# Optimization experiments

Measured on AMD Instinct MI355X. Metric: run time of the kernel, lower is better.

The kernel has to match this reference:

```python
import jax, jax.numpy as jnp
import numpy as np

NUM_HEADS = 8
GROUPS = 32
EPS = 1e-5


def group_norm(x, gamma, beta):
    # x: [B, C, H, W], normalize over (C/G, H, W) per group
    B, C, H, W = x.shape
    xg = x.reshape(B, GROUPS, -1)
    mu = xg.mean(axis=-1, keepdims=True)
    var = xg.var(axis=-1, keepdims=True)
    xg = (xg - mu) * jax.lax.rsqrt(var + EPS)
    x = xg.reshape(B, C, H, W)
    return x * gamma[None, :, None, None] + beta[None, :, None, None]


def reference(x, w_qkv, w_out, b_out, temperature, g1, beta1, g2, beta2,
              w_mlp1, b_mlp1, w_mlp2, b_mlp2):
    B, C, H, W = x.shape
    hd = C // NUM_HEADS
    N = H * W
    identity = x

    xn = group_norm(x, g1, beta1)
    # 1x1 conv == per-pixel matmul
    qkv = jnp.einsum('oc,bchw->bohw', w_qkv, xn)  # [B, 3C, H, W]
    q, k, v = jnp.split(qkv, 3, axis=1)
    q = q.reshape(B, NUM_HEADS, hd, N)
    k = k.reshape(B, NUM_HEADS, hd, N)
    v = v.reshape(B, NUM_HEADS, hd, N)

    temp = jnp.clip(temperature, 1e-4, 10.0)  # [heads,1,1]
    attn = jnp.einsum('bhdi,bhdj->bhij', q, k) * temp[None]  # [B,h,N,N]
    attn = jax.nn.softmax(attn, axis=-1)  # max-subtract is folded into stable softmax

    out = jnp.einsum('bhdj,bhij->bhdi', v, attn)  # [B,h,hd,N]
    out = out.reshape(B, C, H, W)
    out = jnp.einsum('oc,bchw->bohw', w_out, out) + b_out[None, :, None, None]
    x = identity + out

    y = group_norm(x, g2, beta2)
    h = jnp.einsum('oc,bchw->bohw', w_mlp1, y) + b_mlp1[None, :, None, None]
    h = jax.nn.gelu(h, approximate=False)
    m = jnp.einsum('oc,bchw->bohw', w_mlp2, h) + b_mlp2[None, :, None, None]
    return x + m


def setup_inputs() -> dict:
    key = jax.random.key(0)
    ks = jax.random.split(key, 8)
    C = 256
    B, H, W = 2, 64, 64
    hid = C // 4
    s_in = 1.0 / np.sqrt(C)
    s_hid = 1.0 / np.sqrt(hid)
    return {
        'x': jax.random.normal(ks[0], (B, C, H, W), jnp.float32),
        'w_qkv': jax.random.normal(ks[1], (3 * C, C), jnp.float32) * s_in,
        'w_out': jax.random.normal(ks[2], (C, C), jnp.float32) * s_in,
        'b_out': jnp.zeros((C,), jnp.float32),
        'temperature': jnp.ones((NUM_HEADS, 1, 1), jnp.float32) * (C // NUM_HEADS) ** -0.5,
        'g1': jnp.ones((C,), jnp.float32),
        'beta1': jnp.zeros((C,), jnp.float32),
        'g2': jnp.ones((C,), jnp.float32),
        'beta2': jnp.zeros((C,), jnp.float32),
        'w_mlp1': jax.random.normal(ks[3], (hid, C), jnp.float32) * s_in,
        'b_mlp1': jnp.zeros((hid,), jnp.float32),
        'w_mlp2': jax.random.normal(ks[4], (C, hid), jnp.float32) * s_hid,
        'b_mlp2': jnp.zeros((C,), jnp.float32),
    }
```

## Files before the change

### kernel.cpp

```cpp
#include <hip/hip_runtime.h>
#include <hip/hip_bf16.h>
#include <math.h>

#define NB 2
#define NC 256
#define NHEAD 8
#define HD 32
#define NPIX 4096
#define GEPS 1e-5f
#define NCHUNK 2
#define JLEN (NPIX / NCHUNK)

typedef short bf16x8 __attribute__((ext_vector_type(8)));
typedef float f32x4 __attribute__((ext_vector_type(4)));

typedef __attribute__((address_space(3))) unsigned int lds_u32;
typedef __attribute__((address_space(1))) const unsigned int glb_u32;

union U16x8 { uint4 u4; uint2 u2[2]; unsigned u32[4]; unsigned short us[8]; bf16x8 v; };

__device__ inline unsigned short tobf(float f) {
  union { float f; unsigned u; } c; c.f = f;
  return (unsigned short)((c.u + 0x7FFFu + ((c.u >> 16) & 1u)) >> 16);
}
__device__ inline unsigned packtrunc(float lo, float hi) {
  return __builtin_amdgcn_perm(__float_as_uint(hi), __float_as_uint(lo), 0x07060302u);
}
__device__ inline float geluf(float v) {
  return 0.5f * v * (1.f + erff(v * 0.70710678118654752f));
}

__device__ inline int detect_bf(const void* xraw) {
  __shared__ int flg;
  int t = threadIdx.x;
  if (t < 64) {
    unsigned short h = ((const unsigned short*)xraw)[2 * t];
    unsigned e = (h >> 7) & 0xFFu;
    int weird = (e < 113u || e > 140u) ? 1 : 0;
    unsigned long long m = __ballot(weird);
    if (t == 0) flg = (__popcll(m) > 16) ? 0 : 1;
  }
  __syncthreads();
  return flg;
}

struct ConvArgs { const void* src[13]; int off[14]; };

__device__ inline float ldsrc(const void* p, int idx, int bf) {
  if (bf) {
    unsigned v = ((const unsigned short*)p)[idx];
    return __uint_as_float(v << 16);
  }
  return ((const float*)p)[idx];
}

__global__ __launch_bounds__(256) void conv_prep_kernel(
    ConvArgs a, float* __restrict__ dstbase, int total,
    unsigned short* __restrict__ wqkv_b, unsigned short* __restrict__ wout_b,
    unsigned short* __restrict__ wm1_b, unsigned short* __restrict__ wm2_b,
    float* __restrict__ qscale, float* __restrict__ part1p) {
  int bf = detect_bf(a.src[0]);
  int blk = blockIdx.x, t = threadIdx.x;
  int i = blk * 256 + t;
  float val = 0.f;
  if (i < total) {
    int s = 0;
    while (i >= a.off[s + 1]) ++s;
    val = ldsrc(a.src[s], i - a.off[s], bf);
    dstbase[i] = val;
  }
  if (blk < 8192) {
    __shared__ float rs[256], rq[256];
    rs[t] = val;
    rq[t] = val * val;
    __syncthreads();
    for (int o = 128; o > 0; o >>= 1) {
      if (t < o) { rs[t] += rs[t + o]; rq[t] += rq[t + o]; }
      __syncthreads();
    }
    if (t == 0) { part1p[blk * 2] = rs[0]; part1p[blk * 2 + 1] = rq[0]; }
  }
  if (i < 196608) wqkv_b[i] = tobf(ldsrc(a.src[1], i, bf));
  else if (i < 262144) wout_b[i - 196608] = tobf(ldsrc(a.src[2], i - 196608, bf));
  else if (i < 278528) wm1_b[i - 262144] = tobf(ldsrc(a.src[9], i - 262144, bf));
  else if (i < 294912) wm2_b[i - 278528] = tobf(ldsrc(a.src[11], i - 278528, bf));
  if (i < 768) {
    if (i < 256) {
      float tc = fminf(fmaxf(ldsrc(a.src[4], i >> 5, bf), 1e-4f), 10.f);
      qscale[i] = tc * 1.4426950408889634f;
    } else qscale[i] = 1.0f;
  }
}

__global__ __launch_bounds__(256) void qkv_fused_kernel(
    const float* __restrict__ x_f, const float* __restrict__ part1p,
    const float* __restrict__ g1, const float* __restrict__ be1,
    const unsigned short* __restrict__ W, const float* __restrict__ qscale,
    unsigned short* __restrict__ qn, unsigned short* __restrict__ kn,
    unsigned short* __restrict__ vs) {
  int t = threadIdx.x;
  int w = t >> 6, lane = t & 63, l16 = lane & 15, quad = lane >> 4;
  int p0 = blockIdx.x * 16;
  int b = p0 >> 12;
  __shared__ float red[32][8][2];
  __shared__ float sm[32], si[32];
  {
    int g = t >> 3, seg = t & 7;
    float s = 0.f, s2 = 0.f;
    const float* pp = part1p + ((size_t)(b * 32 + g) * 128 + seg * 16) * 2;
#pragma unroll
    for (int k = 0; k < 16; ++k) { s += pp[k * 2]; s2 += pp[k * 2 + 1]; }
    red[g][seg][0] = s; red[g][seg][1] = s2;
  }
  __syncthreads();
  if (t < 32) {
    float s = 0.f, s2 = 0.f;
#pragma unroll
    for (int k = 0; k < 8; ++k) { s += red[t][k][0]; s2 += red[t][k][1]; }
    float mean = s * (1.f / 32768.f);
    float var = s2 * (1.f / 32768.f) - mean * mean;
    sm[t] = mean; si[t] = rsqrtf(var + GEPS);
  }
  __syncthreads();
  __shared__ unsigned short Ys[16][264];
  {
    int p = t & 15, cg = t >> 4;
    int n = (p0 & 4095) + p;
    const float* src = x_f + ((size_t)b * NC + cg * 16) * NPIX + n;
    U16x8 lo, hi;
#pragma unroll
    for (int cc = 0; cc < 16; ++cc) {
      int c = cg * 16 + cc;
      int g = c >> 3;
      float gg = g1[c] * si[g];
      float vv = (src[(size_t)cc * NPIX] - sm[g]) * gg + be1[c];
      if (cc < 8) lo.us[cc] = tobf(vv); else hi.us[cc - 8] = tobf(vv);
    }
    *(uint4*)&Ys[p][cg * 16] = lo.u4;
    *(uint4*)&Ys[p][cg * 16 + 8] = hi.u4;
  }
  __syncthreads();
  int ob = blockIdx.y * 384 + w * 96;
  f32x4 acc[6] = {};
#pragma unroll
  for (int k0 = 0; k0 < 256; k0 += 32) {
    U16x8 bfr; bfr.u4 = *(const uint4*)&Ys[l16][k0 + quad * 8];
#pragma unroll
    for (int ot = 0; ot < 6; ++ot) {
      U16x8 af;
      af.u4 = *(const uint4*)(W + (size_t)(ob + ot * 16 + l16) * 256 + k0 + quad * 8);
      acc[ot] = __builtin_amdgcn_mfma_f32_16x16x32_bf16(af.v, bfr.v, acc[ot], 0, 0, 0);
    }
  }
  int n = (p0 & 4095) + l16;
#pragma unroll
  for (int ot = 0; ot < 6; ++ot) {
    int oc = ob + ot * 16 + quad * 4;
    float v[4];
#pragma unroll
    for (int r = 0; r < 4; ++r) v[r] = acc[ot][r] * qscale[oc + r];
    int sec = oc >> 8;
    int c = oc & 255;
    if (sec < 2) {
      int hh = c >> 5, d = c & 31;
      unsigned short* base = sec == 0 ? qn : kn;
      uint2 pk;
      pk.x = (unsigned)tobf(v[0]) | ((unsigned)tobf(v[1]) << 16);
      pk.y = (unsigned)tobf(v[2]) | ((unsigned)tobf(v[3]) << 16);
      *(uint2*)(base + ((size_t)(b * NHEAD + hh) * NPIX + n) * HD + d) = pk;
    } else {
#pragma unroll
      for (int r = 0; r < 4; ++r)
        vs[((size_t)(b * NC + c + r)) * NPIX + n] = tobf(v[r]);
    }
  }
}

__global__ __launch_bounds__(512) void attn11_kernel(
    const unsigned short* __restrict__ qn, const unsigned short* __restrict__ kn,
    const unsigned short* __restrict__ vs, float* __restrict__ pO,
    float* __restrict__ pl) {
  int f = blockIdx.x;
  int xcd = f & 7, slot = f >> 3;
  int s = xcd + ((slot >> 5) << 3);
  int iblk = slot & 31;
  int chunk = s & 1;
  int h = (s >> 1) & 7;
  int b = s >> 4;
  int i0 = iblk * 128;
  int jbase = chunk * JLEN;
  int bh = b * NHEAD + h;
  int t = threadIdx.x;
  int w = t >> 6, lane = t & 63, l16 = lane & 15, quad = lane >> 4;

  __shared__ unsigned short Kt[2][2048];
  __shared__ unsigned short Vt[2][2048];
  __shared__ unsigned short Pl[8][16][72];

  U16x8 qf;
  qf.u4 = *(const uint4*)(qn + ((size_t)bh * NPIX + i0 + w * 16 + l16) * HD + quad * 8);
  U16x8 ones;
#pragma unroll
  for (int j = 0; j < 8; ++j) ones.us[j] = 0x3F80;

  const unsigned short* gp;
  lds_u32* dstN[2];
  if (w < 4) {
    int kj = (w << 4) + (lane >> 2);
    int kg = (lane & 3) ^ ((kj >> 1) & 3);
    gp = kn + ((size_t)bh * NPIX + jbase + kj) * HD + kg * 8;
    dstN[0] = (lds_u32*)&Kt[0][w * 512];
    dstN[1] = (lds_u32*)&Kt[1][w * 512];
  } else {
    int vd = ((w - 4) << 3) + (lane >> 3);
    int vg = (lane & 7) ^ (vd & 7);
    gp = vs + ((size_t)(b * NC + h * HD + vd)) * NPIX + jbase + vg * 8;
    dstN[0] = (lds_u32*)&Vt[0][(w - 4) * 512];
    dstN[1] = (lds_u32*)&Vt[1][(w - 4) * 512];
  }
  int gstep = (w < 4) ? 64 * HD : 64;

  f32x4 o0 = {0.f, 0.f, 0.f, 0.f}, o1 = {0.f, 0.f, 0.f, 0.f};
  f32x4 lacc = {0.f, 0.f, 0.f, 0.f};
  const f32x4 zf = {0.f, 0.f, 0.f, 0.f};

  int sp = (quad ^ ((l16 >> 1) & 3)) * 8;

  __builtin_amdgcn_global_load_lds((glb_u32*)gp, dstN[0], 16, 0, 0);
  gp += gstep;

#define ATTN_STEP(CUR, ISSUE)                                                   \
  {                                                                             \
    asm volatile("s_waitcnt vmcnt(0)" ::: "memory");                            \
    __builtin_amdgcn_s_barrier();                                               \
    if (ISSUE) {                                                                \
      __builtin_amdgcn_global_load_lds((glb_u32*)gp, dstN[(CUR) ^ 1], 16, 0, 0);\
      gp += gstep;                                                              \
    }                                                                           \
    __builtin_amdgcn_sched_barrier(0);                                          \
    f32x4 st[4];                                                                \
    __builtin_amdgcn_s_setprio(1);                                              \
    _Pragma("unroll")                                                           \
    for (int jj = 0; jj < 4; ++jj) {                                            \
      U16x8 kf; kf.u4 = *(const uint4*)&Kt[CUR][(jj * 16 + l16) * 32 + sp];     \
      st[jj] = __builtin_amdgcn_mfma_f32_16x16x32_bf16(kf.v, qf.v, zf, 0, 0, 0);\
    }                                                                           \
    __builtin_amdgcn_s_setprio(0);                                              \
    _Pragma("unroll")                                                           \
    for (int jj = 0; jj < 4; ++jj) {                                            \
      uint2 pk;                                                                 \
      pk.x = packtrunc(__builtin_amdgcn_exp2f(st[jj][0]),                       \
                       __builtin_amdgcn_exp2f(st[jj][1]));                      \
      pk.y = packtrunc(__builtin_amdgcn_exp2f(st[jj][2]),                       \
                       __builtin_amdgcn_exp2f(st[jj][3]));                      \
      *(uint2*)&Pl[w][l16][jj * 16 + quad * 4] = pk;                            \
    }                                                                           \
    __builtin_amdgcn_s_setprio(1);                                              \
    _Pragma("unroll")                                                           \
    for (int ks = 0; ks < 2; ++ks) {                                            \
      U16x8 pb; pb.u4 = *(const uint4*)&Pl[w][l16][ks * 32 + quad * 8];         \
      int vp = ((ks * 4 + quad) ^ (l16 & 7)) * 8;                               \
      U16x8 va; va.u4 = *(const uint4*)&Vt[CUR][l16 * 64 + vp];                 \
      U16x8 vb2; vb2.u4 = *(const uint4*)&Vt[CUR][(16 + l16) * 64 + vp];        \
      o0 = __builtin_amdgcn_mfma_f32_16x16x32_bf16(va.v, pb.v, o0, 0, 0, 0);    \
      o1 = __builtin_amdgcn_mfma_f32_16x16x32_bf16(vb2.v, pb.v, o1, 0, 0, 0);   \
      lacc = __builtin_amdgcn_mfma_f32_16x16x32_bf16(ones.v, pb.v, lacc, 0, 0, 0);\
    }                                                                           \
    __builtin_amdgcn_s_setprio(0);                                              \
  }

#pragma unroll 1
  for (int it = 0; it < 15; ++it) {
    ATTN_STEP(0, 1)
    ATTN_STEP(1, 1)
  }
  ATTN_STEP(0, 1)
  ATTN_STEP(1, 0)
#undef ATTN_STEP

  int pr = bh * 64 + iblk * 2 + (w >> 2);
  float* ob = pO + ((size_t)chunk * 1024 + pr) * 2048;
  int icol = (w & 3) * 16 + l16;
#pragma unroll
  for (int r = 0; r < 4; ++r) {
    ob[(quad * 4 + r) * 64 + icol] = o0[r];
    ob[(16 + quad * 4 + r) * 64 + icol] = o1[r];
  }
  if (quad == 0)
    pl[((size_t)chunk * 1024 + pr) * 64 + icol] = lacc[0];
}

__global__ __launch_bounds__(256) void wout_kernel(
    const unsigned short* __restrict__ W, const float* __restrict__ pO,
    const float* __restrict__ pl, const float* __restrict__ bias,
    const float* __restrict__ res, float* __restrict__ xres_t,
    float* __restrict__ part2p) {
  int t = threadIdx.x;
  int w = t >> 6, lane = t & 63, l16 = lane & 15, quad = lane >> 4;
  int p = blockIdx.x * 16 + l16;
  int b = p >> 12, n = p & 4095;
  int i = p & 63, iblk = (p >> 6) & 63;
  int ob = w * 64;
  float rinv8[8];
#pragma unroll
  for (int hh = 0; hh < 8; ++hh) {
    size_t pr = (size_t)(b * NHEAD + hh) * 64 + iblk;
    float l = pl[pr * 64 + i] + pl[(1024 + pr) * 64 + i];
    rinv8[hh] = 1.f / l;
  }
  f32x4 acc[4] = {};
#pragma unroll
  for (int k0 = 0; k0 < 256; k0 += 32) {
    int hh = k0 >> 5;
    const float* q0 = pO + ((size_t)(b * NHEAD + hh) * 64 + iblk) * 2048 + quad * 8 * 64 + i;
    const float* q1 = q0 + (size_t)1024 * 2048;
    float rv = rinv8[hh];
    U16x8 bfr;
#pragma unroll
    for (int u = 0; u < 4; ++u) {
      float va = (q0[(2 * u) * 64] + q1[(2 * u) * 64]) * rv;
      float vb = (q0[(2 * u + 1) * 64] + q1[(2 * u + 1) * 64]) * rv;
      bfr.u32[u] = packtrunc(va, vb);
    }
#pragma unroll
    for (int ot = 0; ot < 4; ++ot) {
      U16x8 af;
      af.u4 = *(const uint4*)(W + (size_t)(ob + ot * 16 + l16) * 256 + k0 + quad * 8);
      acc[ot] = __builtin_amdgcn_mfma_f32_16x16x32_bf16(af.v, bfr.v, acc[ot], 0, 0, 0);
    }
  }
  __shared__ float sb[256][4][2];
#pragma unroll
  for (int ot = 0; ot < 4; ++ot) {
    int oc = ob + ot * 16 + quad * 4;
    float s = 0.f, s2 = 0.f;
    float v4[4];
#pragma unroll
    for (int r = 0; r < 4; ++r) {
      float vv = acc[ot][r] + bias[oc + r] + res[((size_t)(b * NC + oc + r)) * NPIX + n];
      v4[r] = vv;
      s += vv; s2 += vv * vv;
    }
    *(float4*)&xres_t[(size_t)p * NC + oc] = make_float4(v4[0], v4[1], v4[2], v4[3]);
    sb[t][ot][0] = s; sb[t][ot][1] = s2;
  }
  __syncthreads();
  if (t < 32) {
    int ww = t >> 3, rem = t & 7, ot = rem >> 1, qp = rem & 1;
    float s = 0.f, s2 = 0.f;
#pragma unroll
    for (int q = 2 * qp; q < 2 * qp + 2; ++q)
      for (int l = 0; l < 16; ++l) {
        int tt = ww * 64 + q * 16 + l;
        s += sb[tt][ot][0]; s2 += sb[tt][ot][1];
      }
    size_t idx = ((size_t)(b * 32 + t) * 256 + (blockIdx.x & 255)) * 2;
    part2p[idx] = s; part2p[idx + 1] = s2;
  }
}

__global__ __launch_bounds__(256) void mlp_fused_kernel(
    const void* __restrict__ xraw, const float* __restrict__ xres_t,
    const float* __restrict__ part2p, const float* __restrict__ g2,
    const float* __restrict__ be2, const unsigned short* __restrict__ W1,
    const float* __restrict__ b1, const unsigned short* __restrict__ W2,
    const float* __restrict__ b2, void* __restrict__ dout) {
  int wbf = detect_bf(xraw);
  int t = threadIdx.x;
  int w = t >> 6, lane = t & 63, l16 = lane & 15, quad = lane >> 4;
  int p0 = blockIdx.x * 16;
  int b = p0 >> 12;
  __shared__ float red[32][8][2];
  __shared__ float sm[32], si[32];
  {
    int g = t >> 3, seg = t & 7;
    float s = 0.f, s2 = 0.f;
    const float* pp = part2p + ((size_t)(b * 32 + g) * 256 + seg * 32) * 2;
#pragma unroll
    for (int k = 0; k < 32; ++k) { s += pp[k * 2]; s2 += pp[k * 2 + 1]; }
    red[g][seg][0] = s; red[g][seg][1] = s2;
  }
  __syncthreads();
  if (t < 32) {
    float s = 0.f, s2 = 0.f;
#pragma unroll
    for (int k = 0; k < 8; ++k) { s += red[t][k][0]; s2 += red[t][k][1]; }
    float mean = s * (1.f / 32768.f);
    float var = s2 * (1.f / 32768.f) - mean * mean;
    sm[t] = mean; si[t] = rsqrtf(var + GEPS);
  }
  __syncthreads();
  __shared__ float Xs[16][261];
  __shared__ unsigned short Ys[16][264];
  {
    int p = t >> 4, cg = t & 15;
    const float* src = xres_t + (size_t)(p0 + p) * NC + cg * 16;
    U16x8 lo, hi;
#pragma unroll
    for (int cc = 0; cc < 16; ++cc) {
      int c = cg * 16 + cc;
      int g = c >> 3;
      float v = src[cc];
      Xs[p][c] = v;
      float yv = (v - sm[g]) * (g2[c] * si[g]) + be2[c];
      if (cc < 8) lo.us[cc] = tobf(yv); else hi.us[cc - 8] = tobf(yv);
    }
    *(uint4*)&Ys[p][cg * 16] = lo.u4;
    *(uint4*)&Ys[p][cg * 16 + 8] = hi.u4;
  }
  __syncthreads();
  f32x4 a1 = {0.f, 0.f, 0.f, 0.f};
#pragma unroll
  for (int k0 = 0; k0 < 256; k0 += 32) {
    U16x8 bfr; bfr.u4 = *(const uint4*)&Ys[l16][k0 + quad * 8];
    U16x8 af;
    af.u4 = *(const uint4*)(W1 + (size_t)(w * 16 + l16) * 256 + k0 + quad * 8);
    a1 = __builtin_amdgcn_mfma_f32_16x16x32_bf16(af.v, bfr.v, a1, 0, 0, 0);
  }
  __shared__ unsigned short Hs[16][72];
  {
    int oc = w * 16 + quad * 4;
    float h0 = geluf(a1[0] + b1[oc]),     h1 = geluf(a1[1] + b1[oc + 1]);
    float h2 = geluf(a1[2] + b1[oc + 2]), h3 = geluf(a1[3] + b1[oc + 3]);
    uint2 pk;
    pk.x = (unsigned)tobf(h0) | ((unsigned)tobf(h1) << 16);
    pk.y = (unsigned)tobf(h2) | ((unsigned)tobf(h3) << 16);
    *(uint2*)&Hs[l16][oc] = pk;
  }
  __syncthreads();
  f32x4 a2[4] = {};
#pragma unroll
  for (int k0 = 0; k0 < 64; k0 += 32) {
    U16x8 bfr; bfr.u4 = *(const uint4*)&Hs[l16][k0 + quad * 8];
#pragma unroll
    for (int ot = 0; ot < 4; ++ot) {
      U16x8 af;
      af.u4 = *(const uint4*)(W2 + (size_t)(w * 64 + ot * 16 + l16) * 64 + k0 + quad * 8);
      a2[ot] = __builtin_amdgcn_mfma_f32_16x16x32_bf16(af.v, bfr.v, a2[ot], 0, 0, 0);
    }
  }
  int n = (p0 & 4095) + l16;
#pragma unroll
  for (int ot = 0; ot < 4; ++ot) {
    int oc = w * 64 + ot * 16 + quad * 4;
#pragma unroll
    for (int r = 0; r < 4; ++r) {
      float v = a2[ot][r] + b2[oc + r] + Xs[l16][oc + r];
      size_t oidx = ((size_t)(b * NC + oc + r)) * NPIX + n;
      if (wbf) ((__hip_bfloat16*)dout)[oidx] = __float2bfloat16(v);
      else ((float*)dout)[oidx] = v;
    }
  }
}

extern "C" void kernel_launch(void* const* d_in, const int* in_sizes, int n_in,
                              void* d_out, int out_size, void* d_ws, size_t ws_size,
                              hipStream_t stream) {
  float* ws = (float*)d_ws;
  size_t off = 16;
  float* x_f    = ws + off; off += (size_t)NB * NC * NPIX;
  float* wqkv_f = ws + off; off += 768 * 256;
  float* wout_f = ws + off; off += 256 * 256;
  float* bout_f = ws + off; off += 256;
  float* temp_f = ws + off; off += 8;
  float* g1_f   = ws + off; off += 256;
  float* be1_f  = ws + off; off += 256;
  float* g2_f   = ws + off; off += 256;
  float* be2_f  = ws + off; off += 256;
  float* wm1_f  = ws + off; off += 64 * 256;
  float* bm1_f  = ws + off; off += 64;
  float* wm2_f  = ws + off; off += 256 * 64;
  float* bm2_f  = ws + off; off += 256;
  float* xres   = ws + off; off += (size_t)NB * NC * NPIX;
  unsigned short* qn     = (unsigned short*)(ws + off); off += 1048576;
  unsigned short* kn     = (unsigned short*)(ws + off); off += 1048576;
  unsigned short* vs     = (unsigned short*)(ws + off); off += 1048576;
  unsigned short* wqkv_b = (unsigned short*)(ws + off); off += 98304;
  unsigned short* wout_b = (unsigned short*)(ws + off); off += 32768;
  unsigned short* wm1_b  = (unsigned short*)(ws + off); off += 8192;
  unsigned short* wm2_b  = (unsigned short*)(ws + off); off += 8192;
  float* qscale = ws + off; off += 768;
  float* part1p = ws + off; off += 16384;
  float* part2p = ws + off; off += 65536;
  float* pO     = ws + off; off += (size_t)NCHUNK * 1024 * 2048;
  float* plb    = ws + off; off += (size_t)NCHUNK * 1024 * 64;
  (void)wqkv_f; (void)wout_f; (void)wm1_f; (void)wm2_f; (void)temp_f; (void)bm1_f;

  ConvArgs ca;
  int acc = 0;
  for (int i = 0; i < 13; ++i) {
    ca.src[i] = d_in[i];
    ca.off[i] = acc;
    acc += (i < n_in) ? in_sizes[i] : 0;
  }
  ca.off[13] = acc;
  conv_prep_kernel<<<(acc + 255) / 256, 256, 0, stream>>>(
      ca, x_f, acc, wqkv_b, wout_b, wm1_b, wm2_b, qscale, part1p);

  qkv_fused_kernel<<<dim3(512, 2), 256, 0, stream>>>(
      x_f, part1p, g1_f, be1_f, wqkv_b, qscale, qn, kn, vs);

  attn11_kernel<<<dim3(1024), 512, 0, stream>>>(qn, kn, vs, pO, plb);

  wout_kernel<<<512, 256, 0, stream>>>(wout_b, pO, plb, bout_f, x_f, xres, part2p);

  mlp_fused_kernel<<<512, 256, 0, stream>>>(
      d_in[0], xres, part2p, g2_f, be2_f, wm1_b, bm1_f, wm2_b, bm2_f, d_out);
}
```

Measured before the change: 210.6 us.

## Software-pipeline attention: overlap QK^T of next tile with PV of previous

Restructures the attention inner loop so each step computes QK^T scores for the current K tile while running the PV MFMAs for the previous tile's probabilities held in registers. K and V loads are staggered by one stage, with K prefetched a tile ahead and V loaded into the current buffer, and an epilogue drains the final PV. The aim is to hide exp2 and pack latency behind matrix work and shorten the dependency chain per step. It adds register pressure from carrying the packed P across iterations and depends on the buffer-index bookkeeping being correct.

```diff
diff --git a/kernel.cpp b/kernel.cpp
--- a/kernel.cpp
+++ b/kernel.cpp
@@ -176,7 +176,7 @@
   }
 }
 
-__global__ __launch_bounds__(512) void attn11_kernel(
+__global__ __launch_bounds__(512) void attn12_kernel(
     const unsigned short* __restrict__ qn, const unsigned short* __restrict__ kn,
     const unsigned short* __restrict__ vs, float* __restrict__ pO,
     float* __restrict__ pl) {
@@ -223,60 +223,83 @@
   f32x4 o0 = {0.f, 0.f, 0.f, 0.f}, o1 = {0.f, 0.f, 0.f, 0.f};
   f32x4 lacc = {0.f, 0.f, 0.f, 0.f};
   const f32x4 zf = {0.f, 0.f, 0.f, 0.f};
+  uint2 pk[4];
 
   int sp = (quad ^ ((l16 >> 1) & 3)) * 8;
 
-  __builtin_amdgcn_global_load_lds((glb_u32*)gp, dstN[0], 16, 0, 0);
-  gp += gstep;
-
-#define ATTN_STEP(CUR, ISSUE)                                                   \
+  if (w < 4) {
+    __builtin_amdgcn_global_load_lds((glb_u32*)gp, dstN[0], 16, 0, 0);
+    gp += gstep;
+  }
+
+#define ATTN_STEP(P, DOPV)                                                      \
   {                                                                             \
     asm volatile("s_waitcnt vmcnt(0)" ::: "memory");                            \
     __builtin_amdgcn_s_barrier();                                               \
-    if (ISSUE) {                                                                \
-      __builtin_amdgcn_global_load_lds((glb_u32*)gp, dstN[(CUR) ^ 1], 16, 0, 0);\
+    {                                                                           \
+      lds_u32* d_ = (w < 4) ? dstN[(P) ^ 1] : dstN[(P)];                        \
+      __builtin_amdgcn_global_load_lds((glb_u32*)gp, d_, 16, 0, 0);             \
       gp += gstep;                                                              \
     }                                                                           \
     __builtin_amdgcn_sched_barrier(0);                                          \
+    if (DOPV) {                                                                 \
+      _Pragma("unroll")                                                         \
+      for (int jj = 0; jj < 4; ++jj)                                            \
+        *(uint2*)&Pl[w][l16][jj * 16 + quad * 4] = pk[jj];                      \
+    }                                                                           \
     f32x4 st[4];                                                                \
     __builtin_amdgcn_s_setprio(1);                                              \
     _Pragma("unroll")                                                           \
     for (int jj = 0; jj < 4; ++jj) {                                            \
-      U16x8 kf; kf.u4 = *(const uint4*)&Kt[CUR][(jj * 16 + l16) * 32 + sp];     \
+      U16x8 kf; kf.u4 = *(const uint4*)&Kt[P][(jj * 16 + l16) * 32 + sp];       \
       st[jj] = __builtin_amdgcn_mfma_f32_16x16x32_bf16(kf.v, qf.v, zf, 0, 0, 0);\
+    }                                                                           \
+    if (DOPV) {                                                                 \
+      _Pragma("unroll")                                                         \
+      for (int ks = 0; ks < 2; ++ks) {                                          \
+        U16x8 pb; pb.u4 = *(const uint4*)&Pl[w][l16][ks * 32 + quad * 8];       \
+        int vp = ((ks * 4 + quad) ^ (l16 & 7)) * 8;                             \
+        U16x8 va; va.u4 = *(const uint4*)&Vt[(P) ^ 1][l16 * 64 + vp];           \
+        U16x8 vb2; vb2.u4 = *(const uint4*)&Vt[(P) ^ 1][(16 + l16) * 64 + vp];  \
+        o0 = __builtin_amdgcn_mfma_f32_16x16x32_bf16(va.v, pb.v, o0, 0, 0, 0);  \
+        o1 = __builtin_amdgcn_mfma_f32_16x16x32_bf16(vb2.v, pb.v, o1, 0, 0, 0); \
+        lacc = __builtin_amdgcn_mfma_f32_16x16x32_bf16(ones.v, pb.v, lacc, 0, 0, 0);\
+      }                                                                         \
     }                                                                           \
     __builtin_amdgcn_s_setprio(0);                                              \
     _Pragma("unroll")                                                           \
     for (int jj = 0; jj < 4; ++jj) {                                            \
-      uint2 pk;                                                                 \
-      pk.x = packtrunc(__builtin_amdgcn_exp2f(st[jj][0]),                       \
-                       __builtin_amdgcn_exp2f(st[jj][1]));                      \
-      pk.y = packtrunc(__builtin_amdgcn_exp2f(st[jj][2]),                       \
-                       __builtin_amdgcn_exp2f(st[jj][3]));                      \
-      *(uint2*)&Pl[w][l16][jj * 16 + quad * 4] = pk;                            \
+      pk[jj].x = packtrunc(__builtin_amdgcn_exp2f(st[jj][0]),                   \
+                           __builtin_amdgcn_exp2f(st[jj][1]));                  \
+      pk[jj].y = packtrunc(__builtin_amdgcn_exp2f(st[jj][2]),                   \
+                           __builtin_amdgcn_exp2f(st[jj][3]));                  \
     }                                                                           \
-    __builtin_amdgcn_s_setprio(1);                                              \
-    _Pragma("unroll")                                                           \
-    for (int ks = 0; ks < 2; ++ks) {                                            \
-      U16x8 pb; pb.u4 = *(const uint4*)&Pl[w][l16][ks * 32 + quad * 8];         \
-      int vp = ((ks * 4 + quad) ^ (l16 & 7)) * 8;                               \
-      U16x8 va; va.u4 = *(const uint4*)&Vt[CUR][l16 * 64 + vp];                 \
-      U16x8 vb2; vb2.u4 = *(const uint4*)&Vt[CUR][(16 + l16) * 64 + vp];        \
-      o0 = __builtin_amdgcn_mfma_f32_16x16x32_bf16(va.v, pb.v, o0, 0, 0, 0);    \
-      o1 = __builtin_amdgcn_mfma_f32_16x16x32_bf16(vb2.v, pb.v, o1, 0, 0, 0);   \
-      lacc = __builtin_amdgcn_mfma_f32_16x16x32_bf16(ones.v, pb.v, lacc, 0, 0, 0);\
-    }                                                                           \
-    __builtin_amdgcn_s_setprio(0);                                              \
-  }
-
+  }
+
+  ATTN_STEP(0, 0)
+  ATTN_STEP(1, 1)
 #pragma unroll 1
   for (int it = 0; it < 15; ++it) {
     ATTN_STEP(0, 1)
     ATTN_STEP(1, 1)
   }
-  ATTN_STEP(0, 1)
-  ATTN_STEP(1, 0)
 #undef ATTN_STEP
+
+  asm volatile("s_waitcnt vmcnt(0)" ::: "memory");
+  __builtin_amdgcn_s_barrier();
+#pragma unroll
+  for (int jj = 0; jj < 4; ++jj)
+    *(uint2*)&Pl[w][l16][jj * 16 + quad * 4] = pk[jj];
+#pragma unroll
+  for (int ks = 0; ks < 2; ++ks) {
+    U16x8 pb; pb.u4 = *(const uint4*)&Pl[w][l16][ks * 32 + quad * 8];
+    int vp = ((ks * 4 + quad) ^ (l16 & 7)) * 8;
+    U16x8 va; va.u4 = *(const uint4*)&Vt[1][l16 * 64 + vp];
+    U16x8 vb2; vb2.u4 = *(const uint4*)&Vt[1][(16 + l16) * 64 + vp];
+    o0 = __builtin_amdgcn_mfma_f32_16x16x32_bf16(va.v, pb.v, o0, 0, 0, 0);
+    o1 = __builtin_amdgcn_mfma_f32_16x16x32_bf16(vb2.v, pb.v, o1, 0, 0, 0);
+    lacc = __builtin_amdgcn_mfma_f32_16x16x32_bf16(ones.v, pb.v, lacc, 0, 0, 0);
+  }
 
   int pr = bh * 64 + iblk * 2 + (w >> 2);
   float* ob = pO + ((size_t)chunk * 1024 + pr) * 2048;
@@ -500,7 +523,7 @@
   qkv_fused_kernel<<<dim3(512, 2), 256, 0, stream>>>(
       x_f, part1p, g1_f, be1_f, wqkv_b, qscale, qn, kn, vs);
 
-  attn11_kernel<<<dim3(1024), 512, 0, stream>>>(qn, kn, vs, pO, plb);
+  attn12_kernel<<<dim3(1024), 512, 0, stream>>>(qn, kn, vs, pO, plb);
 
   wout_kernel<<<512, 256, 0, stream>>>(wout_b, pO, plb, bout_f, x_f, xres, part2p);
 
```

New measurement: 211.5 us. No clear change (+0.4%).

## Rewrite attention with 32x32x16 MFMA and register-resident P via permlane swap

Applied to the files above, without the earlier changes.

The attention kernel moves from 16x16x32 MFMA tiles with 8 waves to 32x32x16 MFMA tiles with 4 waves, each wave covering 32 query rows. The softmax probabilities are now converted in registers with v_permlane32_swap instead of being written to and read back from an LDS staging buffer, which removes the Pl shared array and its LDS traffic. K and V loads are now issued by every wave rather than split between wave groups. The trade-offs are fewer waves per block, higher register pressure from the 16-wide accumulators, and a new LDS access pattern without the previous XOR swizzle, which may cause bank conflicts.

```diff
diff --git a/kernel.cpp b/kernel.cpp
--- a/kernel.cpp
+++ b/kernel.cpp
@@ -13,6 +13,7 @@
 
 typedef short bf16x8 __attribute__((ext_vector_type(8)));
 typedef float f32x4 __attribute__((ext_vector_type(4)));
+typedef float f32x16 __attribute__((ext_vector_type(16)));
 
 typedef __attribute__((address_space(3))) unsigned int lds_u32;
 typedef __attribute__((address_space(1))) const unsigned int glb_u32;
@@ -28,6 +29,9 @@
 }
 __device__ inline float geluf(float v) {
   return 0.5f * v * (1.f + erff(v * 0.70710678118654752f));
+}
+__device__ inline void plane32(unsigned &a, unsigned &b) {
+  asm("v_permlane32_swap_b32 %0, %1" : "+v"(a), "+v"(b));
 }
 
 __device__ inline int detect_bf(const void* xraw) {
@@ -176,7 +180,7 @@
   }
 }
 
-__global__ __launch_bounds__(512) void attn11_kernel(
+__global__ __launch_bounds__(256) void attn15_kernel(
     const unsigned short* __restrict__ qn, const unsigned short* __restrict__ kn,
     const unsigned short* __restrict__ vs, float* __restrict__ pO,
     float* __restrict__ pl) {
@@ -191,80 +195,102 @@
   int jbase = chunk * JLEN;
   int bh = b * NHEAD + h;
   int t = threadIdx.x;
-  int w = t >> 6, lane = t & 63, l16 = lane & 15, quad = lane >> 4;
+  int w = t >> 6, lane = t & 63;
+  int q = lane & 31, lh = lane >> 5;
 
   __shared__ unsigned short Kt[2][2048];
   __shared__ unsigned short Vt[2][2048];
-  __shared__ unsigned short Pl[8][16][72];
-
-  U16x8 qf;
-  qf.u4 = *(const uint4*)(qn + ((size_t)bh * NPIX + i0 + w * 16 + l16) * HD + quad * 8);
+
+  int px = i0 + w * 32 + q;
+  U16x8 qf0, qf1;
+  qf0.u4 = *(const uint4*)(qn + ((size_t)bh * NPIX + px) * HD + lh * 8);
+  qf1.u4 = *(const uint4*)(qn + ((size_t)bh * NPIX + px) * HD + 16 + lh * 8);
   U16x8 ones;
 #pragma unroll
   for (int j = 0; j < 8; ++j) ones.us[j] = 0x3F80;
 
-  const unsigned short* gp;
-  lds_u32* dstN[2];
-  if (w < 4) {
-    int kj = (w << 4) + (lane >> 2);
-    int kg = (lane & 3) ^ ((kj >> 1) & 3);
-    gp = kn + ((size_t)bh * NPIX + jbase + kj) * HD + kg * 8;
-    dstN[0] = (lds_u32*)&Kt[0][w * 512];
-    dstN[1] = (lds_u32*)&Kt[1][w * 512];
-  } else {
-    int vd = ((w - 4) << 3) + (lane >> 3);
-    int vg = (lane & 7) ^ (vd & 7);
-    gp = vs + ((size_t)(b * NC + h * HD + vd)) * NPIX + jbase + vg * 8;
-    dstN[0] = (lds_u32*)&Vt[0][(w - 4) * 512];
-    dstN[1] = (lds_u32*)&Vt[1][(w - 4) * 512];
-  }
-  int gstep = (w < 4) ? 64 * HD : 64;
-
-  f32x4 o0 = {0.f, 0.f, 0.f, 0.f}, o1 = {0.f, 0.f, 0.f, 0.f};
-  f32x4 lacc = {0.f, 0.f, 0.f, 0.f};
-  const f32x4 zf = {0.f, 0.f, 0.f, 0.f};
-
-  int sp = (quad ^ ((l16 >> 1) & 3)) * 8;
-
-  __builtin_amdgcn_global_load_lds((glb_u32*)gp, dstN[0], 16, 0, 0);
-  gp += gstep;
+  const unsigned short* gpk = kn + ((size_t)bh * NPIX + jbase + lane) * HD + w * 8;
+  const unsigned short* gpv =
+      vs + ((size_t)(b * NC + h * HD + q)) * NPIX + jbase + (2 * w + lh) * 8;
+  lds_u32* dstK[2] = {(lds_u32*)&Kt[0][w * 512], (lds_u32*)&Kt[1][w * 512]};
+  lds_u32* dstV[2] = {(lds_u32*)&Vt[0][w * 512], (lds_u32*)&Vt[1][w * 512]};
+
+  f32x16 O = {};
+  f32x16 lacc = {};
+  const f32x16 zf16 = {};
+
+  __builtin_amdgcn_global_load_lds((glb_u32*)gpk, dstK[0], 16, 0, 0);
+  gpk += 64 * HD;
+  __builtin_amdgcn_global_load_lds((glb_u32*)gpv, dstV[0], 16, 0, 0);
+  gpv += 64;
+
+#define SOFT2(ST, PA, PB)                                                       \
+  {                                                                             \
+    unsigned Xa = packtrunc(__builtin_amdgcn_exp2f(ST[0]),                      \
+                            __builtin_amdgcn_exp2f(ST[1]));                     \
+    unsigned Za = packtrunc(__builtin_amdgcn_exp2f(ST[4]),                      \
+                            __builtin_amdgcn_exp2f(ST[5]));                     \
+    unsigned Ya = packtrunc(__builtin_amdgcn_exp2f(ST[2]),                      \
+                            __builtin_amdgcn_exp2f(ST[3]));                     \
+    unsigned Wa = packtrunc(__builtin_amdgcn_exp2f(ST[6]),                      \
+                            __builtin_amdgcn_exp2f(ST[7]));                     \
+    plane32(Xa, Za); plane32(Ya, Wa);                                           \
+    PA.u32[0] = Xa; PA.u32[1] = Ya; PA.u32[2] = Za; PA.u32[3] = Wa;             \
+    unsigned Xb = packtrunc(__builtin_amdgcn_exp2f(ST[8]),                      \
+                            __builtin_amdgcn_exp2f(ST[9]));                     \
+    unsigned Zb = packtrunc(__builtin_amdgcn_exp2f(ST[12]),                     \
+                            __builtin_amdgcn_exp2f(ST[13]));                    \
+    unsigned Yb = packtrunc(__builtin_amdgcn_exp2f(ST[10]),                     \
+                            __builtin_amdgcn_exp2f(ST[11]));                    \
+    unsigned Wb = packtrunc(__builtin_amdgcn_exp2f(ST[14]),                     \
+                            __builtin_amdgcn_exp2f(ST[15]));                    \
+    plane32(Xb, Zb); plane32(Yb, Wb);                                           \
+    PB.u32[0] = Xb; PB.u32[1] = Yb; PB.u32[2] = Zb; PB.u32[3] = Wb;             \
+  }
 
 #define ATTN_STEP(CUR, ISSUE)                                                   \
   {                                                                             \
     asm volatile("s_waitcnt vmcnt(0)" ::: "memory");                            \
     __builtin_amdgcn_s_barrier();                                               \
     if (ISSUE) {                                                                \
-      __builtin_amdgcn_global_load_lds((glb_u32*)gp, dstN[(CUR) ^ 1], 16, 0, 0);\
-      gp += gstep;                                                              \
+      __builtin_amdgcn_global_load_lds((glb_u32*)gpk, dstK[(CUR) ^ 1], 16, 0, 0);\
+      gpk += 64 * HD;                                                           \
+      __builtin_amdgcn_global_load_lds((glb_u32*)gpv, dstV[(CUR) ^ 1], 16, 0, 0);\
+      gpv += 64;                                                                \
     }                                                                           \
     __builtin_amdgcn_sched_barrier(0);                                          \
-    f32x4 st[4];                                                                \
+    f32x16 stA, stB;                                                            \
     __builtin_amdgcn_s_setprio(1);                                              \
-    _Pragma("unroll")                                                           \
-    for (int jj = 0; jj < 4; ++jj) {                                            \
-      U16x8 kf; kf.u4 = *(const uint4*)&Kt[CUR][(jj * 16 + l16) * 32 + sp];     \
-      st[jj] = __builtin_amdgcn_mfma_f32_16x16x32_bf16(kf.v, qf.v, zf, 0, 0, 0);\
+    {                                                                           \
+      U16x8 k0, k1, k2, k3;                                                     \
+      k0.u4 = *(const uint4*)&Kt[CUR][lh * 512 + q * 8];                        \
+      k1.u4 = *(const uint4*)&Kt[CUR][(2 + lh) * 512 + q * 8];                  \
+      k2.u4 = *(const uint4*)&Kt[CUR][lh * 512 + 256 + q * 8];                  \
+      k3.u4 = *(const uint4*)&Kt[CUR][(2 + lh) * 512 + 256 + q * 8];            \
+      stA = __builtin_amdgcn_mfma_f32_32x32x16_bf16(k0.v, qf0.v, zf16, 0, 0, 0);\
+      stA = __builtin_amdgcn_mfma_f32_32x32x16_bf16(k1.v, qf1.v, stA, 0, 0, 0); \
+      stB = __builtin_amdgcn_mfma_f32_32x32x16_bf16(k2.v, qf0.v, zf16, 0, 0, 0);\
+      stB = __builtin_amdgcn_mfma_f32_32x32x16_bf16(k3.v, qf1.v, stB, 0, 0, 0); \
     }                                                                           \
     __builtin_amdgcn_s_setprio(0);                                              \
-    _Pragma("unroll")                                                           \
-    for (int jj = 0; jj < 4; ++jj) {                                            \
-      uint2 pk;                                                                 \
-      pk.x = packtrunc(__builtin_amdgcn_exp2f(st[jj][0]),                       \
-                       __builtin_amdgcn_exp2f(st[jj][1]));                      \
-      pk.y = packtrunc(__builtin_amdgcn_exp2f(st[jj][2]),                       \
-                       __builtin_amdgcn_exp2f(st[jj][3]));                      \
-      *(uint2*)&Pl[w][l16][jj * 16 + quad * 4] = pk;                            \
-    }                                                                           \
+    U16x8 P1, P2, P3, P4;                                                       \
+    SOFT2(stA, P1, P2)                                                          \
+    SOFT2(stB, P3, P4)                                                          \
     __builtin_amdgcn_s_setprio(1);                                              \
-    _Pragma("unroll")                                                           \
-    for (int ks = 0; ks < 2; ++ks) {                                            \
-      U16x8 pb; pb.u4 = *(const uint4*)&Pl[w][l16][ks * 32 + quad * 8];         \
-      int vp = ((ks * 4 + quad) ^ (l16 & 7)) * 8;                               \
-      U16x8 va; va.u4 = *(const uint4*)&Vt[CUR][l16 * 64 + vp];                 \
-      U16x8 vb2; vb2.u4 = *(const uint4*)&Vt[CUR][(16 + l16) * 64 + vp];        \
-      o0 = __builtin_amdgcn_mfma_f32_16x16x32_bf16(va.v, pb.v, o0, 0, 0, 0);    \
-      o1 = __builtin_amdgcn_mfma_f32_16x16x32_bf16(vb2.v, pb.v, o1, 0, 0, 0);   \
-      lacc = __builtin_amdgcn_mfma_f32_16x16x32_bf16(ones.v, pb.v, lacc, 0, 0, 0);\
+    {                                                                           \
+      U16x8 v0, v1, v2, v3;                                                     \
+      v0.u4 = *(const uint4*)&Vt[CUR][lh * 256 + q * 8];                        \
+      v1.u4 = *(const uint4*)&Vt[CUR][(2 + lh) * 256 + q * 8];                  \
+      v2.u4 = *(const uint4*)&Vt[CUR][(4 + lh) * 256 + q * 8];                  \
+      v3.u4 = *(const uint4*)&Vt[CUR][(6 + lh) * 256 + q * 8];                  \
+      O = __builtin_amdgcn_mfma_f32_32x32x16_bf16(v0.v, P1.v, O, 0, 0, 0);      \
+      lacc = __builtin_amdgcn_mfma_f32_32x32x16_bf16(ones.v, P1.v, lacc, 0, 0, 0);\
+      O = __builtin_amdgcn_mfma_f32_32x32x16_bf16(v1.v, P2.v, O, 0, 0, 0);      \
+      lacc = __builtin_amdgcn_mfma_f32_32x32x16_bf16(ones.v, P2.v, lacc, 0, 0, 0);\
+      O = __builtin_amdgcn_mfma_f32_32x32x16_bf16(v2.v, P3.v, O, 0, 0, 0);      \
+      lacc = __builtin_amdgcn_mfma_f32_32x32x16_bf16(ones.v, P3.v, lacc, 0, 0, 0);\
+      O = __builtin_amdgcn_mfma_f32_32x32x16_bf16(v3.v, P4.v, O, 0, 0, 0);      \
+      lacc = __builtin_amdgcn_mfma_f32_32x32x16_bf16(ones.v, P4.v, lacc, 0, 0, 0);\
     }                                                                           \
     __builtin_amdgcn_s_setprio(0);                                              \
   }
@@ -277,17 +303,18 @@
   ATTN_STEP(0, 1)
   ATTN_STEP(1, 0)
 #undef ATTN_STEP
-
-  int pr = bh * 64 + iblk * 2 + (w >> 2);
+#undef SOFT2
+
+  int pr = bh * 64 + iblk * 2 + (w >> 1);
   float* ob = pO + ((size_t)chunk * 1024 + pr) * 2048;
-  int icol = (w & 3) * 16 + l16;
-#pragma unroll
-  for (int r = 0; r < 4; ++r) {
-    ob[(quad * 4 + r) * 64 + icol] = o0[r];
-    ob[(16 + quad * 4 + r) * 64 + icol] = o1[r];
-  }
-  if (quad == 0)
-    pl[((size_t)chunk * 1024 + pr) * 64 + icol] = lacc[0];
+  int col = (w & 1) * 32 + q;
+#pragma unroll
+  for (int r = 0; r < 16; ++r) {
+    int d = (r & 3) + 8 * (r >> 2) + 4 * lh;
+    ob[d * 64 + col] = O[r];
+  }
+  if (lane < 32)
+    pl[((size_t)chunk * 1024 + pr) * 64 + col] = lacc[0];
 }
 
 __global__ __launch_bounds__(256) void wout_kernel(
@@ -500,7 +527,7 @@
   qkv_fused_kernel<<<dim3(512, 2), 256, 0, stream>>>(
       x_f, part1p, g1_f, be1_f, wqkv_b, qscale, qn, kn, vs);
 
-  attn11_kernel<<<dim3(1024), 512, 0, stream>>>(qn, kn, vs, pO, plb);
+  attn15_kernel<<<dim3(1024), 256, 0, stream>>>(qn, kn, vs, pO, plb);
 
   wout_kernel<<<512, 256, 0, stream>>>(wout_b, pO, plb, bout_f, x_f, xres, part2p);
 
```

Result: slower. 226.8 us (+7.7%).
